# Kernel optimization log

Measured on AMD Instinct MI355X. Metric: run time of the kernel, lower is better.

## Reference

```python
import jax, jax.numpy as jnp
import numpy as np

CLASSES = (32, 32)
SUPERCLASSES = 8
OVERALL = CLASSES[0] * CLASSES[1]
CLASS_FACTOR = OVERALL // SUPERCLASSES


def lrelu(x):
    return jax.nn.leaky_relu(x, 0.01)


def conv1x1(x, w, b):
    # x: [B,C,H,W], w: [O,C], b: [O]
    return jnp.einsum('oc,bchw->bohw', w, x) + b[None, :, None, None]


def cond_mul(x, inds, W, b):
    # x: [N,I], inds: [N] int, W: [K,I,O], b: [K,O]
    return jnp.einsum('ni,nio->no', x, W[inds]) + b[inds]


def setup_inputs() -> dict:
    key = jax.random.key(0)
    ks = jax.random.split(key, 24)
    s = 0.05
    d = {}
    d['x_in'] = jax.random.normal(ks[0], (1, 128, 192, 256), dtype=jnp.float32)
    # mask branch
    d['Wm1'] = jax.random.normal(ks[1], (32, 128)) * s
    d['bm1'] = jnp.zeros((32,), jnp.float32)
    d['Wm2'] = jax.random.normal(ks[2], (16, 32)) * s
    d['bm2'] = jnp.zeros((16,), jnp.float32)
    d['Wm3'] = jax.random.normal(ks[3], (1, 16)) * s
    d['bm3'] = jnp.zeros((1,), jnp.float32)
    # classification branch
    d['Wcl1'] = jax.random.normal(ks[4], (128, 128)) * s
    d['bcl1'] = jnp.zeros((128,), jnp.float32)
    d['Wcl21'] = jax.random.normal(ks[5], (128, 128)) * s
    d['bcl21'] = jnp.zeros((128,), jnp.float32)
    d['Wcl31'] = jax.random.normal(ks[6], (32, 128)) * s
    d['bcl31'] = jnp.zeros((32,), jnp.float32)
    d['Wcl22'] = jax.random.normal(ks[7], (CLASSES[0], 128, 32)) * s  # CondMul
    d['bcl22'] = jnp.zeros((CLASSES[0], 32), jnp.float32)
    d['Wcl32'] = jax.random.normal(ks[8], (CLASSES[0], 32, CLASSES[1])) * s
    d['bcl32'] = jnp.zeros((CLASSES[0], CLASSES[1]), jnp.float32)
    d['Wr1'] = jax.random.normal(ks[9], (128, 128)) * s
    d['br1'] = jnp.zeros((128,), jnp.float32)
    d['Wr2'] = jax.random.normal(ks[10], (SUPERCLASSES, 128, 32)) * s
    d['br2'] = jnp.zeros((SUPERCLASSES, 32), jnp.float32)
    d['Wr3'] = jax.random.normal(ks[11], (OVERALL, 32, 1)) * s
    d['br3'] = jnp.zeros((OVERALL, 1), jnp.float32)
    return d


def reference(x_in, Wm1, bm1, Wm2, bm2, Wm3, bm3,
              Wcl1, bcl1, Wcl21, bcl21, Wcl31, bcl31,
              Wcl22, bcl22, Wcl32, bcl32,
              Wr1, br1, Wr2, br2, Wr3, br3):
    B = x_in.shape[0]
    # mask branch
    m = lrelu(conv1x1(x_in, Wm1, bm1))
    m = lrelu(conv1x1(m, Wm2, bm2))
    mask = lrelu(conv1x1(m, Wm3, bm3))
    # classification branch
    x = lrelu(conv1x1(x_in, Wcl1, bcl1))          # [B,128,H,W]
    # torch: transpose(1,3) -> [B,W,H,C], flatten
    x_l = jnp.transpose(x, (0, 3, 2, 1)).reshape(-1, x.shape[1])
    x2 = lrelu(conv1x1(x, Wcl21, bcl21))
    cl1 = conv1x1(x2, Wcl31, bcl31)               # [B,classes0,H,W]
    inds1 = jnp.argmax(cl1, axis=1).reshape(-1).astype(jnp.int32)  # [N] (B,H,W order)
    h = lrelu(cond_mul(x_l, inds1, Wcl22, bcl22))  # [N,32]
    h = cond_mul(h, inds1, Wcl32, bcl32)           # [N,classes1]
    inds2 = jnp.argmax(h, axis=1).astype(jnp.int32)
    inds = inds1 * CLASSES[1] + inds2
    inds_r = jnp.clip(inds, 0, OVERALL - 1).astype(jnp.int32)
    inds_super = jnp.clip(inds_r // CLASS_FACTOR, 0, SUPERCLASSES - 1)
    r = lrelu(conv1x1(x_in, Wr1, br1))
    r_l = jnp.transpose(r, (0, 3, 2, 1)).reshape(-1, r.shape[1])
    r2 = lrelu(cond_mul(r_l, inds_super, Wr2, br2))  # [N,32]
    regression = cond_mul(r2, inds_r, Wr3, br3)      # [N,1]
    regression = regression.reshape(B, 1, 1, -1)
    inds = inds.reshape(regression.shape)
    x_real = (inds.astype(jnp.float32) + regression) * (1.0 / float(OVERALL))
    return (x_real, mask)
```

## Files before the change

### kernel.cpp

```cpp
#include <hip/hip_runtime.h>

#define HH 192
#define WW 256
#define NPIX (HH*WW)
#define NSEG (NPIX/64)

__device__ __forceinline__ float lrelu(float v) { return v > 0.0f ? v : 0.01f * v; }

__global__ __launch_bounds__(256, 3) void k_fused1(
    const float* __restrict__ X,
    const float* __restrict__ Wcl1, const float* __restrict__ bcl1,
    const float* __restrict__ Wr1,  const float* __restrict__ br1,
    const float* __restrict__ Wm1,  const float* __restrict__ bm1,
    const float* __restrict__ Wm2,  const float* __restrict__ bm2,
    const float* __restrict__ Wm3,  const float* __restrict__ bm3,
    float* __restrict__ x_t, float* __restrict__ r_t,
    float* __restrict__ out)
{
    __shared__ float As[16][132];
    __shared__ float Ws[16][132];
    __shared__ float m1buf[128][33];
    const int tid = threadIdx.x;
    const int q0  = blockIdx.x * 128;

    if (blockIdx.y == 2) {
        const int tc = tid & 31;
        const int tr = tid >> 5;
        float acc[4][4];
        #pragma unroll
        for (int i = 0; i < 4; ++i)
            #pragma unroll
            for (int j = 0; j < 4; ++j)
                acc[i][j] = bm1[tr * 4 + j];

        for (int k0 = 0; k0 < 128; k0 += 16) {
            #pragma unroll
            for (int p = 0; p < 2; ++p) {
                int lin = p * 1024 + tid * 4;
                int kk = lin >> 7, px = lin & 127;
                float4 v = *(const float4*)(X + (k0 + kk) * NPIX + q0 + px);
                *(float4*)(&As[kk][px]) = v;
            }
            if (tid < 128) {
                int row = tid >> 2, kc = (tid & 3) * 4;
                float4 v = *(const float4*)(Wm1 + row * 128 + k0 + kc);
                Ws[kc + 0][row] = v.x; Ws[kc + 1][row] = v.y;
                Ws[kc + 2][row] = v.z; Ws[kc + 3][row] = v.w;
            }
            __syncthreads();
            #pragma unroll
            for (int kk = 0; kk < 16; ++kk) {
                float4 a = *(const float4*)(&As[kk][tc * 4]);
                float4 w = *(const float4*)(&Ws[kk][tr * 4]);
                float av[4] = {a.x,a.y,a.z,a.w};
                float wv[4] = {w.x,w.y,w.z,w.w};
                #pragma unroll
                for (int i = 0; i < 4; ++i)
                    #pragma unroll
                    for (int j = 0; j < 4; ++j)
                        acc[i][j] = fmaf(av[i], wv[j], acc[i][j]);
            }
            __syncthreads();
        }
        #pragma unroll
        for (int i = 0; i < 4; ++i)
            #pragma unroll
            for (int j = 0; j < 4; ++j)
                m1buf[tc * 4 + i][tr * 4 + j] = lrelu(acc[i][j]);
        __syncthreads();
        if (tid < 128) {
            float m3 = bm3[0];
            #pragma unroll 2
            for (int j = 0; j < 16; ++j) {
                float s = bm2[j];
                #pragma unroll
                for (int k = 0; k < 32; ++k)
                    s = fmaf(Wm2[j * 32 + k], m1buf[tid][k], s);
                m3 = fmaf(Wm3[j], lrelu(s), m3);
            }
            out[NPIX + q0 + tid] = lrelu(m3);
        }
        return;
    }

    const float* __restrict__ W    = (blockIdx.y == 0) ? Wcl1 : Wr1;
    const float* __restrict__ bias = (blockIdx.y == 0) ? bcl1 : br1;
    float* __restrict__ outp       = (blockIdx.y == 0) ? x_t : r_t;

    const int tc = tid & 15;
    const int tr = tid >> 4;

    float acc[8][8];
    #pragma unroll
    for (int i = 0; i < 8; ++i)
        #pragma unroll
        for (int j = 0; j < 8; ++j)
            acc[i][j] = bias[(j >> 2) * 64 + tr * 4 + (j & 3)];

    for (int k0 = 0; k0 < 128; k0 += 16) {
        #pragma unroll
        for (int p = 0; p < 2; ++p) {
            int lin = p * 1024 + tid * 4;
            int kk = lin >> 7, px = lin & 127;
            float4 v = *(const float4*)(X + (k0 + kk) * NPIX + q0 + px);
            *(float4*)(&As[kk][px]) = v;
        }
        #pragma unroll
        for (int p = 0; p < 2; ++p) {
            int lin = p * 1024 + tid * 4;
            int row = lin >> 4, kc = lin & 15;
            float4 v = *(const float4*)(W + row * 128 + k0 + kc);
            Ws[kc + 0][row] = v.x; Ws[kc + 1][row] = v.y;
            Ws[kc + 2][row] = v.z; Ws[kc + 3][row] = v.w;
        }
        __syncthreads();
        #pragma unroll
        for (int kk = 0; kk < 16; ++kk) {
            float4 a0 = *(const float4*)(&As[kk][tc * 4]);
            float4 a1 = *(const float4*)(&As[kk][64 + tc * 4]);
            float4 w0 = *(const float4*)(&Ws[kk][tr * 4]);
            float4 w1 = *(const float4*)(&Ws[kk][64 + tr * 4]);
            float av[8] = {a0.x,a0.y,a0.z,a0.w,a1.x,a1.y,a1.z,a1.w};
            float wv[8] = {w0.x,w0.y,w0.z,w0.w,w1.x,w1.y,w1.z,w1.w};
            #pragma unroll
            for (int i = 0; i < 8; ++i)
                #pragma unroll
                for (int j = 0; j < 8; ++j)
                    acc[i][j] = fmaf(av[i], wv[j], acc[i][j]);
        }
        __syncthreads();
    }

    #pragma unroll
    for (int i = 0; i < 8; ++i) {
        int px = (i >> 2) * 64 + tc * 4 + (i & 3);
        int q  = q0 + px;
        int np = (q & 255) * 192 + (q >> 8);
        float* op = outp + (size_t)np * 128;
        #pragma unroll
        for (int jg = 0; jg < 2; ++jg) {
            float4 o;
            o.x = lrelu(acc[i][jg*4+0]); o.y = lrelu(acc[i][jg*4+1]);
            o.z = lrelu(acc[i][jg*4+2]); o.w = lrelu(acc[i][jg*4+3]);
            *(float4*)(op + jg * 64 + tr * 4) = o;
        }
    }
}

__global__ __launch_bounds__(256, 2) void k1b(
    const float* __restrict__ x_t,
    const float* __restrict__ Wcl21, const float* __restrict__ bcl21,
    const float* __restrict__ Wcl31, const float* __restrict__ bcl31,
    int* __restrict__ inds1_q)
{
    __shared__ float smem[12672];
    float (*As)[132]     = (float(*)[132])smem;
    float (*Ws)[132]     = (float(*)[132])(smem + 2112);
    float (*W31)[132]    = (float(*)[132])smem;
    float (*x2t)[132]    = (float(*)[132])(smem + 4224);
    float (*cl1buf)[33]  = (float(*)[33]) (smem + 4224);

    const int tid = threadIdx.x;
    const int n0  = blockIdx.x * 128;
    const int tcA = tid & 15, trA = tid >> 4;
    const int tcB = tid & 31, trB = tid >> 5;

    float accB[4][4];
    #pragma unroll
    for (int i = 0; i < 4; ++i)
        #pragma unroll
        for (int j = 0; j < 4; ++j)
            accB[i][j] = bcl31[trB * 4 + j];

    for (int h = 0; h < 2; ++h) {
        float acc2[2][4][4];
        #pragma unroll
        for (int gi = 0; gi < 2; ++gi)
            #pragma unroll
            for (int i = 0; i < 4; ++i)
                #pragma unroll
                for (int j = 0; j < 4; ++j)
                    acc2[gi][i][j] = bcl21[h * 64 + trA * 4 + j];

        for (int k0 = 0; k0 < 128; k0 += 16) {
            #pragma unroll
            for (int p = 0; p < 2; ++p) {
                int lin = p * 1024 + tid * 4;
                int px = lin >> 4, kc = lin & 15;
                float4 v = *(const float4*)(x_t + (size_t)(n0 + px) * 128 + k0 + kc);
                As[kc + 0][px] = v.x; As[kc + 1][px] = v.y;
                As[kc + 2][px] = v.z; As[kc + 3][px] = v.w;
            }
            {
                int r = tid >> 2, kc = (tid & 3) * 4;
                float4 v = *(const float4*)(Wcl21 + (h * 64 + r) * 128 + k0 + kc);
                Ws[kc + 0][r] = v.x; Ws[kc + 1][r] = v.y;
                Ws[kc + 2][r] = v.z; Ws[kc + 3][r] = v.w;
            }
            __syncthreads();
            #pragma unroll
            for (int kk = 0; kk < 16; ++kk) {
                float4 a0 = *(const float4*)(&As[kk][tcA * 4]);
                float4 a1 = *(const float4*)(&As[kk][64 + tcA * 4]);
                float4 w  = *(const float4*)(&Ws[kk][trA * 4]);
                float av0[4] = {a0.x,a0.y,a0.z,a0.w};
                float av1[4] = {a1.x,a1.y,a1.z,a1.w};
                float wv[4]  = {w.x,w.y,w.z,w.w};
                #pragma unroll
                for (int i = 0; i < 4; ++i)
                    #pragma unroll
                    for (int j = 0; j < 4; ++j) {
                        acc2[0][i][j] = fmaf(av0[i], wv[j], acc2[0][i][j]);
                        acc2[1][i][j] = fmaf(av1[i], wv[j], acc2[1][i][j]);
                    }
            }
            __syncthreads();
        }
        #pragma unroll
        for (int j = 0; j < 4; ++j) {
            int row = trA * 4 + j;
            #pragma unroll
            for (int gi = 0; gi < 2; ++gi) {
                float4 o;
                o.x = lrelu(acc2[gi][0][j]); o.y = lrelu(acc2[gi][1][j]);
                o.z = lrelu(acc2[gi][2][j]); o.w = lrelu(acc2[gi][3][j]);
                *(float4*)(&x2t[row][gi * 64 + tcA * 4]) = o;
            }
        }
        __syncthreads();
        #pragma unroll
        for (int p = 0; p < 4; ++p) {
            int lin = p * 1024 + tid * 4;
            int row = lin >> 7, kc = lin & 127;
            *(float4*)(&W31[row][kc]) = *(const float4*)(Wcl31 + row * 128 + kc);
        }
        __syncthreads();
        for (int k = 0; k < 64; ++k) {
            float4 a = *(const float4*)(&x2t[k][tcB * 4]);
            float av[4] = {a.x,a.y,a.z,a.w};
            float wv[4];
            #pragma unroll
            for (int j = 0; j < 4; ++j) wv[j] = W31[trB * 4 + j][h * 64 + k];
            #pragma unroll
            for (int i = 0; i < 4; ++i)
                #pragma unroll
                for (int j = 0; j < 4; ++j)
                    accB[i][j] = fmaf(av[i], wv[j], accB[i][j]);
        }
        __syncthreads();
    }

    #pragma unroll
    for (int i = 0; i < 4; ++i)
        #pragma unroll
        for (int j = 0; j < 4; ++j)
            cl1buf[tcB * 4 + i][trB * 4 + j] = accB[i][j];
    __syncthreads();
    if (tid < 128) {
        float bv = cl1buf[tid][0]; int bi = 0;
        #pragma unroll
        for (int c = 1; c < 32; ++c) {
            float v = cl1buf[tid][c];
            if (v > bv) { bv = v; bi = c; }
        }
        int n = n0 + tid;
        int w = n / 192, hh = n - w * 192;
        inds1_q[hh * 256 + w] = bi;
    }
}

__global__ void k_hist(const int* __restrict__ inds1_q, int* __restrict__ bh) {
    int tid = threadIdx.x;
    int n = blockIdx.x * 256 + tid;
    int key = inds1_q[n];
    int lane = tid & 63;
    int cnt = 0;
    for (int k = 0; k < 32; ++k) {
        unsigned long long m = __ballot(key == k);
        if (lane == k) cnt = __popcll(m);
    }
    if (lane < 32) bh[(n >> 6) * 32 + lane] = cnt;
}

__global__ void k_scanA(const int* __restrict__ bh, int* __restrict__ ebb,
                        int* __restrict__ total) {
    __shared__ int s[256];
    const int k = blockIdx.x, t = threadIdx.x;
    int v0 = bh[(t * 3 + 0) * 32 + k];
    int v1 = bh[(t * 3 + 1) * 32 + k];
    int v2 = bh[(t * 3 + 2) * 32 + k];
    int sum = v0 + v1 + v2;
    s[t] = sum; __syncthreads();
    for (int d = 1; d < 256; d <<= 1) {
        int x = (t >= d) ? s[t - d] : 0;
        __syncthreads();
        s[t] += x;
        __syncthreads();
    }
    int ex = s[t] - sum;
    ebb[(t * 3 + 0) * 32 + k] = ex;
    ebb[(t * 3 + 1) * 32 + k] = ex + v0;
    ebb[(t * 3 + 2) * 32 + k] = ex + v0 + v1;
    if (t == 255) total[k] = s[255];
}

__global__ void k_scatter2(const int* __restrict__ inds1_q,
                           const int* __restrict__ ebb,
                           const int* __restrict__ total,
                           int* __restrict__ order)
{
    __shared__ int ttot[32];
    const int tid = threadIdx.x;
    if (tid < 32) ttot[tid] = total[tid];
    __syncthreads();
    int n = blockIdx.x * 256 + tid;
    int key = inds1_q[n];
    int lane = tid & 63;
    unsigned long long peers = 0;
    for (int k = 0; k < 32; ++k) {
        unsigned long long m = __ballot(key == k);
        if (key == k) peers = m;
    }
    int rank = __popcll(peers & ((1ull << lane) - 1ull));
    int cbase = 0;
    #pragma unroll
    for (int k = 0; k < 32; ++k) cbase += (k < key) ? ttot[k] : 0;
    order[cbase + ebb[(n >> 6) * 32 + key] + rank] = n;
}

__global__ __launch_bounds__(256, 4) void k2h(
    const float* __restrict__ x_t,
    const float* __restrict__ Wcl22, const float* __restrict__ bcl22,
    const float* __restrict__ Wcl32, const float* __restrict__ bcl32,
    const int* __restrict__ total, const int* __restrict__ order,
    int* __restrict__ ind_ord)
{
    __shared__ float Was[4096];
    __shared__ float Wbs[1024];
    __shared__ int cpre[33];
    __shared__ int cbase[33];
    __shared__ int ttot[32];

    const int tid = threadIdx.x;
    if (tid < 32) ttot[tid] = total[tid];
    __syncthreads();
    if (tid == 0) {
        int s = 0, cb = 0;
        for (int k = 0; k < 32; ++k) {
            cpre[k] = s; cbase[k] = cb;
            int c = ttot[k];
            s += (c + 255) >> 8;
            cb += c;
        }
        cpre[32] = s; cbase[32] = cb;
    }
    __syncthreads();
    const int ci = blockIdx.x;
    if (ci >= cpre[32]) return;
    int cls = 0;
    while (cpre[cls + 1] <= ci) ++cls;
    const int st   = (ci - cpre[cls]) * 256;
    const int npx  = min(256, ttot[cls] - st);
    const int base = cbase[cls] + st;

    {
        const float4* ws = (const float4*)(Wcl22 + cls * 4096);
        #pragma unroll
        for (int j = 0; j < 4; ++j) ((float4*)Was)[j * 256 + tid] = ws[j * 256 + tid];
        ((float4*)Wbs)[tid] = ((const float4*)(Wcl32 + cls * 1024))[tid];
    }
    __syncthreads();

    const int m = order[base + min(tid, npx - 1)];
    const float4* xp = (const float4*)(x_t + (size_t)m * 128);

    float h[32];
    #pragma unroll
    for (int j = 0; j < 32; ++j) h[j] = bcl22[cls * 32 + j];
    #pragma unroll 2
    for (int c4 = 0; c4 < 32; ++c4) {
        float4 xv = xp[c4];
        float xa[4] = {xv.x, xv.y, xv.z, xv.w};
        #pragma unroll
        for (int cc = 0; cc < 4; ++cc) {
            const float* wr = &Was[(c4 * 4 + cc) * 32];
            #pragma unroll
            for (int j = 0; j < 32; ++j) h[j] = fmaf(xa[cc], wr[j], h[j]);
        }
    }
    #pragma unroll
    for (int j = 0; j < 32; ++j) h[j] = lrelu(h[j]);

    float g[32];
    #pragma unroll
    for (int j = 0; j < 32; ++j) g[j] = bcl32[cls * 32 + j];
    #pragma unroll 2
    for (int c = 0; c < 32; ++c) {
        float hv = h[c];
        const float* wr = &Wbs[c * 32];
        #pragma unroll
        for (int j = 0; j < 32; ++j) g[j] = fmaf(hv, wr[j], g[j]);
    }
    float bv = g[0]; int bi = 0;
    #pragma unroll
    for (int j = 1; j < 32; ++j)
        if (g[j] > bv) { bv = g[j]; bi = j; }
    if (tid < npx) ind_ord[base + tid] = cls * 32 + bi;
}

__global__ __launch_bounds__(256, 4) void k2r(
    const float* __restrict__ r_t,
    const float* __restrict__ Wr2,  const float* __restrict__ br2,
    const float* __restrict__ Wr3,  const float* __restrict__ br3,
    const int* __restrict__ total, const int* __restrict__ order,
    const int* __restrict__ ind_ord,
    float* __restrict__ out)
{
    __shared__ float Wcs[4096];
    __shared__ int cpre[33];
    __shared__ int cbase[33];
    __shared__ int ttot[32];

    const int tid = threadIdx.x;
    if (tid < 32) ttot[tid] = total[tid];
    __syncthreads();
    if (tid == 0) {
        int s = 0, cb = 0;
        for (int k = 0; k < 32; ++k) {
            cpre[k] = s; cbase[k] = cb;
            int c = ttot[k];
            s += (c + 255) >> 8;
            cb += c;
        }
        cpre[32] = s; cbase[32] = cb;
    }
    __syncthreads();
    const int ci = blockIdx.x;
    if (ci >= cpre[32]) return;
    int cls = 0;
    while (cpre[cls + 1] <= ci) ++cls;
    const int st   = (ci - cpre[cls]) * 256;
    const int npx  = min(256, ttot[cls] - st);
    const int base = cbase[cls] + st;
    const int sup  = cls >> 2;

    {
        const float4* ws = (const float4*)(Wr2 + sup * 4096);
        #pragma unroll
        for (int j = 0; j < 4; ++j) ((float4*)Wcs)[j * 256 + tid] = ws[j * 256 + tid];
    }
    __syncthreads();

    const int li  = min(tid, npx - 1);
    const int m   = order[base + li];
    const int ind = ind_ord[base + li];
    const float4* rp = (const float4*)(r_t + (size_t)m * 128);

    float r2[32];
    #pragma unroll
    for (int j = 0; j < 32; ++j) r2[j] = br2[sup * 32 + j];
    #pragma unroll 2
    for (int c4 = 0; c4 < 32; ++c4) {
        float4 rv = rp[c4];
        float ra[4] = {rv.x, rv.y, rv.z, rv.w};
        #pragma unroll
        for (int cc = 0; cc < 4; ++cc) {
            const float* wr = &Wcs[(c4 * 4 + cc) * 32];
            #pragma unroll
            for (int j = 0; j < 32; ++j) r2[j] = fmaf(ra[cc], wr[j], r2[j]);
        }
    }

    float reg = br3[ind];
    const float* __restrict__ w3 = Wr3 + ind * 32;
    #pragma unroll
    for (int j = 0; j < 32; ++j) reg = fmaf(lrelu(r2[j]), w3[j], reg);

    if (tid < npx) out[m] = ((float)ind + reg) * (1.0f / 1024.0f);
}

extern "C" void kernel_launch(void* const* d_in, const int* in_sizes, int n_in,
                              void* d_out, int out_size, void* d_ws, size_t ws_size,
                              hipStream_t stream)
{
    const float* X     = (const float*)d_in[0];
    const float* Wm1   = (const float*)d_in[1];
    const float* bm1   = (const float*)d_in[2];
    const float* Wm2   = (const float*)d_in[3];
    const float* bm2   = (const float*)d_in[4];
    const float* Wm3   = (const float*)d_in[5];
    const float* bm3   = (const float*)d_in[6];
    const float* Wcl1  = (const float*)d_in[7];
    const float* bcl1  = (const float*)d_in[8];
    const float* Wcl21 = (const float*)d_in[9];
    const float* bcl21 = (const float*)d_in[10];
    const float* Wcl31 = (const float*)d_in[11];
    const float* bcl31 = (const float*)d_in[12];
    const float* Wcl22 = (const float*)d_in[13];
    const float* bcl22 = (const float*)d_in[14];
    const float* Wcl32 = (const float*)d_in[15];
    const float* bcl32 = (const float*)d_in[16];
    const float* Wr1   = (const float*)d_in[17];
    const float* br1   = (const float*)d_in[18];
    const float* Wr2   = (const float*)d_in[19];
    const float* br2   = (const float*)d_in[20];
    const float* Wr3   = (const float*)d_in[21];
    const float* br3   = (const float*)d_in[22];
    float* out = (float*)d_out;

    float* x_t   = (float*)d_ws;
    float* r_t   = x_t + (size_t)NPIX * 128;
    int* inds1_q = (int*)(r_t + (size_t)NPIX * 128);
    int* order   = inds1_q + NPIX;
    int* ind_ord = order + NPIX;
    int* bh      = ind_ord + NPIX;
    int* ebb     = bh + NSEG * 32;
    int* total   = ebb + NSEG * 32;

    k_fused1<<<dim3(NPIX / 128, 3), 256, 0, stream>>>(X, Wcl1, bcl1, Wr1, br1,
                                                      Wm1, bm1, Wm2, bm2, Wm3, bm3,
                                                      x_t, r_t, out);
    k1b<<<NPIX / 128, 256, 0, stream>>>(x_t, Wcl21, bcl21, Wcl31, bcl31, inds1_q);
    k_hist<<<NPIX / 256, 256, 0, stream>>>(inds1_q, bh);
    k_scanA<<<32, 256, 0, stream>>>(bh, ebb, total);
    k_scatter2<<<NPIX / 256, 256, 0, stream>>>(inds1_q, ebb, total, order);
    k2h<<<224, 256, 0, stream>>>(x_t, Wcl22, bcl22, Wcl32, bcl32, total, order, ind_ord);
    k2r<<<224, 256, 0, stream>>>(r_t, Wr2, br2, Wr3, br3, total, order, ind_ord, out);
}
```

Baseline: 246.3 us.

## Double-buffer fused conv GEMM tiles and merge classification/regression tail kernels

Measured after the change: 860.2 us. +249.2%, slower.

```diff
diff --git a/kernel.cpp b/kernel.cpp
--- a/kernel.cpp
+++ b/kernel.cpp
@@ -17,9 +17,13 @@
     float* __restrict__ x_t, float* __restrict__ r_t,
     float* __restrict__ out)
 {
-    __shared__ float As[16][132];
-    __shared__ float Ws[16][132];
-    __shared__ float m1buf[128][33];
+    __shared__ float smem[8448];
+    float (*A0)[132]  = (float(*)[132])(smem);
+    float (*A1)[132]  = (float(*)[132])(smem + 2112);
+    float (*W0)[132]  = (float(*)[132])(smem + 4224);
+    float (*W1)[132]  = (float(*)[132])(smem + 6336);
+    float (*m1buf)[33] = (float(*)[33])(smem + 2112);
+
     const int tid = threadIdx.x;
     const int q0  = blockIdx.x * 128;
 
@@ -38,20 +42,20 @@
             for (int p = 0; p < 2; ++p) {
                 int lin = p * 1024 + tid * 4;
                 int kk = lin >> 7, px = lin & 127;
-                float4 v = *(const float4*)(X + (k0 + kk) * NPIX + q0 + px);
-                *(float4*)(&As[kk][px]) = v;
+                float4 v = *(const float4*)(X + (size_t)(k0 + kk) * NPIX + q0 + px);
+                *(float4*)(&A0[kk][px]) = v;
             }
             if (tid < 128) {
                 int row = tid >> 2, kc = (tid & 3) * 4;
                 float4 v = *(const float4*)(Wm1 + row * 128 + k0 + kc);
-                Ws[kc + 0][row] = v.x; Ws[kc + 1][row] = v.y;
-                Ws[kc + 2][row] = v.z; Ws[kc + 3][row] = v.w;
+                W0[kc + 0][row] = v.x; W0[kc + 1][row] = v.y;
+                W0[kc + 2][row] = v.z; W0[kc + 3][row] = v.w;
             }
             __syncthreads();
             #pragma unroll
             for (int kk = 0; kk < 16; ++kk) {
-                float4 a = *(const float4*)(&As[kk][tc * 4]);
-                float4 w = *(const float4*)(&Ws[kk][tr * 4]);
+                float4 a = *(const float4*)(&A0[kk][tc * 4]);
+                float4 w = *(const float4*)(&W0[kk][tr * 4]);
                 float av[4] = {a.x,a.y,a.z,a.w};
                 float wv[4] = {w.x,w.y,w.z,w.w};
                 #pragma unroll
@@ -90,6 +94,17 @@
     const int tc = tid & 15;
     const int tr = tid >> 4;
 
+    const int lin0 = tid * 4,        lin1 = 1024 + tid * 4;
+    const int akk0 = lin0 >> 7, apx0 = lin0 & 127;
+    const int akk1 = lin1 >> 7, apx1 = lin1 & 127;
+    const int wr0  = lin0 >> 4, wkc0 = lin0 & 15;
+    const int wr1_ = lin1 >> 4, wkc1 = lin1 & 15;
+
+    const float* Xp0 = X + (size_t)akk0 * NPIX + q0 + apx0;
+    const float* Xp1 = X + (size_t)akk1 * NPIX + q0 + apx1;
+    const float* Wp0 = W + wr0  * 128 + wkc0;
+    const float* Wp1 = W + wr1_ * 128 + wkc1;
+
     float acc[8][8];
     #pragma unroll
     for (int i = 0; i < 8; ++i)
@@ -97,29 +112,35 @@
         for (int j = 0; j < 8; ++j)
             acc[i][j] = bias[(j >> 2) * 64 + tr * 4 + (j & 3)];
 
+    float (*Ac)[132] = A0; float (*An)[132] = A1;
+    float (*Wc)[132] = W0; float (*Wn)[132] = W1;
+
+    float4 ra0 = *(const float4*)(Xp0);
+    float4 ra1 = *(const float4*)(Xp1);
+    float4 rw0 = *(const float4*)(Wp0);
+    float4 rw1 = *(const float4*)(Wp1);
+    *(float4*)(&Ac[akk0][apx0]) = ra0;
+    *(float4*)(&Ac[akk1][apx1]) = ra1;
+    Wc[wkc0 + 0][wr0 ] = rw0.x; Wc[wkc0 + 1][wr0 ] = rw0.y;
+    Wc[wkc0 + 2][wr0 ] = rw0.z; Wc[wkc0 + 3][wr0 ] = rw0.w;
+    Wc[wkc1 + 0][wr1_] = rw1.x; Wc[wkc1 + 1][wr1_] = rw1.y;
+    Wc[wkc1 + 2][wr1_] = rw1.z; Wc[wkc1 + 3][wr1_] = rw1.w;
+    __syncthreads();
+
+    #pragma unroll 2
     for (int k0 = 0; k0 < 128; k0 += 16) {
-        #pragma unroll
-        for (int p = 0; p < 2; ++p) {
-            int lin = p * 1024 + tid * 4;
-            int kk = lin >> 7, px = lin & 127;
-            float4 v = *(const float4*)(X + (k0 + kk) * NPIX + q0 + px);
-            *(float4*)(&As[kk][px]) = v;
-        }
-        #pragma unroll
-        for (int p = 0; p < 2; ++p) {
-            int lin = p * 1024 + tid * 4;
-            int row = lin >> 4, kc = lin & 15;
-            float4 v = *(const float4*)(W + row * 128 + k0 + kc);
-            Ws[kc + 0][row] = v.x; Ws[kc + 1][row] = v.y;
-            Ws[kc + 2][row] = v.z; Ws[kc + 3][row] = v.w;
-        }
-        __syncthreads();
+        if (k0 < 112) {
+            ra0 = *(const float4*)(Xp0 + (size_t)(k0 + 16) * NPIX);
+            ra1 = *(const float4*)(Xp1 + (size_t)(k0 + 16) * NPIX);
+            rw0 = *(const float4*)(Wp0 + (k0 + 16));
+            rw1 = *(const float4*)(Wp1 + (k0 + 16));
+        }
         #pragma unroll
         for (int kk = 0; kk < 16; ++kk) {
-            float4 a0 = *(const float4*)(&As[kk][tc * 4]);
-            float4 a1 = *(const float4*)(&As[kk][64 + tc * 4]);
-            float4 w0 = *(const float4*)(&Ws[kk][tr * 4]);
-            float4 w1 = *(const float4*)(&Ws[kk][64 + tr * 4]);
+            float4 a0 = *(const float4*)(&Ac[kk][tc * 4]);
+            float4 a1 = *(const float4*)(&Ac[kk][64 + tc * 4]);
+            float4 w0 = *(const float4*)(&Wc[kk][tr * 4]);
+            float4 w1 = *(const float4*)(&Wc[kk][64 + tr * 4]);
             float av[8] = {a0.x,a0.y,a0.z,a0.w,a1.x,a1.y,a1.z,a1.w};
             float wv[8] = {w0.x,w0.y,w0.z,w0.w,w1.x,w1.y,w1.z,w1.w};
             #pragma unroll
@@ -128,7 +149,18 @@
                 for (int j = 0; j < 8; ++j)
                     acc[i][j] = fmaf(av[i], wv[j], acc[i][j]);
         }
-        __syncthreads();
+        if (k0 < 112) {
+            *(float4*)(&An[akk0][apx0]) = ra0;
+            *(float4*)(&An[akk1][apx1]) = ra1;
+            Wn[wkc0 + 0][wr0 ] = rw0.x; Wn[wkc0 + 1][wr0 ] = rw0.y;
+            Wn[wkc0 + 2][wr0 ] = rw0.z; Wn[wkc0 + 3][wr0 ] = rw0.w;
+            Wn[wkc1 + 0][wr1_] = rw1.x; Wn[wkc1 + 1][wr1_] = rw1.y;
+            Wn[wkc1 + 2][wr1_] = rw1.z; Wn[wkc1 + 3][wr1_] = rw1.w;
+        }
+        __syncthreads();
+        float (*t)[132];
+        t = Ac; Ac = An; An = t;
+        t = Wc; Wc = Wn; Wn = t;
     }
 
     #pragma unroll
@@ -328,15 +360,18 @@
     order[cbase + ebb[(n >> 6) * 32 + key] + rank] = n;
 }
 
-__global__ __launch_bounds__(256, 4) void k2h(
-    const float* __restrict__ x_t,
+__global__ __launch_bounds__(256, 4) void k2hr(
+    const float* __restrict__ x_t, const float* __restrict__ r_t,
     const float* __restrict__ Wcl22, const float* __restrict__ bcl22,
     const float* __restrict__ Wcl32, const float* __restrict__ bcl32,
+    const float* __restrict__ Wr2,  const float* __restrict__ br2,
+    const float* __restrict__ Wr3,  const float* __restrict__ br3,
     const int* __restrict__ total, const int* __restrict__ order,
-    int* __restrict__ ind_ord)
+    float* __restrict__ out)
 {
     __shared__ float Was[4096];
     __shared__ float Wbs[1024];
+    __shared__ float Wcs[4096];
     __shared__ int cpre[33];
     __shared__ int cbase[33];
     __shared__ int ttot[32];
@@ -362,16 +397,22 @@
     const int st   = (ci - cpre[cls]) * 256;
     const int npx  = min(256, ttot[cls] - st);
     const int base = cbase[cls] + st;
+    const int sup  = cls >> 2;
 
     {
-        const float4* ws = (const float4*)(Wcl22 + cls * 4096);
-        #pragma unroll
-        for (int j = 0; j < 4; ++j) ((float4*)Was)[j * 256 + tid] = ws[j * 256 + tid];
+        const float4* wa = (const float4*)(Wcl22 + cls * 4096);
+        const float4* wc = (const float4*)(Wr2 + sup * 4096);
+        #pragma unroll
+        for (int j = 0; j < 4; ++j) {
+            ((float4*)Was)[j * 256 + tid] = wa[j * 256 + tid];
+            ((float4*)Wcs)[j * 256 + tid] = wc[j * 256 + tid];
+        }
         ((float4*)Wbs)[tid] = ((const float4*)(Wcl32 + cls * 1024))[tid];
     }
     __syncthreads();
 
-    const int m = order[base + min(tid, npx - 1)];
+    const int li = min(tid, npx - 1);
+    const int m  = order[base + li];
     const float4* xp = (const float4*)(x_t + (size_t)m * 128);
 
     float h[32];
@@ -405,57 +446,9 @@
     #pragma unroll
     for (int j = 1; j < 32; ++j)
         if (g[j] > bv) { bv = g[j]; bi = j; }
-    if (tid < npx) ind_ord[base + tid] = cls * 32 + bi;
-}
-
-__global__ __launch_bounds__(256, 4) void k2r(
-    const float* __restrict__ r_t,
-    const float* __restrict__ Wr2,  const float* __restrict__ br2,
-    const float* __restrict__ Wr3,  const float* __restrict__ br3,
-    const int* __restrict__ total, const int* __restrict__ order,
-    const int* __restrict__ ind_ord,
-    float* __restrict__ out)
-{
-    __shared__ float Wcs[4096];
-    __shared__ int cpre[33];
-    __shared__ int cbase[33];
-    __shared__ int ttot[32];
-
-    const int tid = threadIdx.x;
-    if (tid < 32) ttot[tid] = total[tid];
-    __syncthreads();
-    if (tid == 0) {
-        int s = 0, cb = 0;
-        for (int k = 0; k < 32; ++k) {
-            cpre[k] = s; cbase[k] = cb;
-            int c = ttot[k];
-            s += (c + 255) >> 8;
-            cb += c;
-        }
-        cpre[32] = s; cbase[32] = cb;
-    }
-    __syncthreads();
-    const int ci = blockIdx.x;
-    if (ci >= cpre[32]) return;
-    int cls = 0;
-    while (cpre[cls + 1] <= ci) ++cls;
-    const int st   = (ci - cpre[cls]) * 256;
-    const int npx  = min(256, ttot[cls] - st);
-    const int base = cbase[cls] + st;
-    const int sup  = cls >> 2;
-
-    {
-        const float4* ws = (const float4*)(Wr2 + sup * 4096);
-        #pragma unroll
-        for (int j = 0; j < 4; ++j) ((float4*)Wcs)[j * 256 + tid] = ws[j * 256 + tid];
-    }
-    __syncthreads();
-
-    const int li  = min(tid, npx - 1);
-    const int m   = order[base + li];
-    const int ind = ind_ord[base + li];
+    const int ind = cls * 32 + bi;
+
     const float4* rp = (const float4*)(r_t + (size_t)m * 128);
-
     float r2[32];
     #pragma unroll
     for (int j = 0; j < 32; ++j) r2[j] = br2[sup * 32 + j];
@@ -524,6 +517,6 @@
     k_hist<<<NPIX / 256, 256, 0, stream>>>(inds1_q, bh);
     k_scanA<<<32, 256, 0, stream>>>(bh, ebb, total);
     k_scatter2<<<NPIX / 256, 256, 0, stream>>>(inds1_q, ebb, total, order);
-    k2h<<<224, 256, 0, stream>>>(x_t, Wcl22, bcl22, Wcl32, bcl32, total, order, ind_ord);
-    k2r<<<224, 256, 0, stream>>>(r_t, Wr2, br2, Wr3, br3, total, order, ind_ord, out);
-}
+    k2hr<<<224, 256, 0, stream>>>(x_t, r_t, Wcl22, bcl22, Wcl32, bcl32,
+                                  Wr2, br2, Wr3, br3, total, order, out);
+}
```

## Double-buffer k_fused1 tiles with direct global-to-LDS async loads

Applied to the files above, without the earlier changes.

Result: slower. 513.7 us (+108.6%).

```diff
diff --git a/kernel.cpp b/kernel.cpp
--- a/kernel.cpp
+++ b/kernel.cpp
@@ -7,66 +7,145 @@
 
 __device__ __forceinline__ float lrelu(float v) { return v > 0.0f ? v : 0.01f * v; }
 
+#define GAS1(p) (const __attribute__((address_space(1))) void*)(p)
+#define LAS3(p) (__attribute__((address_space(3))) void*)(p)
+
+__global__ void k_tw(const float* __restrict__ Wc, const float* __restrict__ Wr,
+                     const float* __restrict__ Wm,
+                     float* __restrict__ Wct, float* __restrict__ Wrt,
+                     float* __restrict__ Wmt)
+{
+    const int b = blockIdx.x, tid = threadIdx.x;
+    const float* __restrict__ src = (b == 0) ? Wc : (b == 1) ? Wr : Wm;
+    float* __restrict__ dst       = (b == 0) ? Wct : (b == 1) ? Wrt : Wmt;
+    const int olog = (b == 2) ? 5 : 7;
+    const int n    = 128 << olog;
+    for (int idx = tid; idx < n; idx += 256) {
+        int k = idx >> olog, o = idx & ((1 << olog) - 1);
+        dst[idx] = src[o * 128 + k];
+    }
+}
+
 __global__ __launch_bounds__(256, 3) void k_fused1(
     const float* __restrict__ X,
-    const float* __restrict__ Wcl1, const float* __restrict__ bcl1,
-    const float* __restrict__ Wr1,  const float* __restrict__ br1,
-    const float* __restrict__ Wm1,  const float* __restrict__ bm1,
+    const float* __restrict__ Wct,  const float* __restrict__ bcl1,
+    const float* __restrict__ Wrt,  const float* __restrict__ br1,
+    const float* __restrict__ Wmt,  const float* __restrict__ bm1,
     const float* __restrict__ Wm2,  const float* __restrict__ bm2,
     const float* __restrict__ Wm3,  const float* __restrict__ bm3,
     float* __restrict__ x_t, float* __restrict__ r_t,
     float* __restrict__ out)
 {
-    __shared__ float As[16][132];
-    __shared__ float Ws[16][132];
-    __shared__ float m1buf[128][33];
+    __shared__ float smem[8192];
+    float (*As0)[128] = (float(*)[128])(smem);
+    float (*Ws0)[128] = (float(*)[128])(smem + 2048);
+    float (*As1)[128] = (float(*)[128])(smem + 4096);
+    float (*Ws1)[128] = (float(*)[128])(smem + 6144);
+    float (*m1buf)[33] = (float(*)[33])smem;
+
     const int tid = threadIdx.x;
+    const int l   = tid & 63;
+    const int wv  = tid >> 6;
     const int q0  = blockIdx.x * 128;
 
+#define STAGE_MAIN(Ab, Wb, Wsrc, kb) do {                                     \
+    int c_ = 2 * wv;                                                          \
+    int row0_ = 2 * c_ + (l >> 5);                                            \
+    int col_  = (l & 31) * 4;                                                 \
+    __builtin_amdgcn_global_load_lds(                                         \
+        GAS1(X + (size_t)((kb) + row0_) * NPIX + q0 + col_),                  \
+        LAS3(&Ab[0][0] + c_ * 256), 16, 0, 0);                                \
+    __builtin_amdgcn_global_load_lds(                                         \
+        GAS1(Wsrc + ((kb) + row0_) * 128 + col_),                             \
+        LAS3(&Wb[0][0] + c_ * 256), 16, 0, 0);                                \
+    int row1_ = row0_ + 2;                                                    \
+    __builtin_amdgcn_global_load_lds(                                         \
+        GAS1(X + (size_t)((kb) + row1_) * NPIX + q0 + col_),                  \
+        LAS3(&Ab[0][0] + c_ * 256 + 256), 16, 0, 0);                          \
+    __builtin_amdgcn_global_load_lds(                                         \
+        GAS1(Wsrc + ((kb) + row1_) * 128 + col_),                             \
+        LAS3(&Wb[0][0] + c_ * 256 + 256), 16, 0, 0);                          \
+} while (0)
+
+#define COMPUTE_MAIN(Ab, Wb) do {                                             \
+    _Pragma("unroll")                                                         \
+    for (int kk = 0; kk < 16; ++kk) {                                         \
+        float4 a0 = *(const float4*)(&Ab[kk][tc * 4]);                        \
+        float4 a1 = *(const float4*)(&Ab[kk][64 + tc * 4]);                   \
+        float4 w0 = *(const float4*)(&Wb[kk][tr * 4]);                        \
+        float4 w1 = *(const float4*)(&Wb[kk][64 + tr * 4]);                   \
+        float av[8] = {a0.x,a0.y,a0.z,a0.w,a1.x,a1.y,a1.z,a1.w};              \
+        float wvv[8] = {w0.x,w0.y,w0.z,w0.w,w1.x,w1.y,w1.z,w1.w};             \
+        _Pragma("unroll")                                                     \
+        for (int i = 0; i < 8; ++i)                                           \
+            _Pragma("unroll")                                                 \
+            for (int j = 0; j < 8; ++j)                                       \
+                acc[i][j] = fmaf(av[i], wvv[j], acc[i][j]);                   \
+    }                                                                         \
+} while (0)
+
     if (blockIdx.y == 2) {
-        const int tc = tid & 31;
-        const int tr = tid >> 5;
-        float acc[4][4];
+        float (*Wm0)[32] = (float(*)[32])(smem + 2048);
+        float (*Wm1b)[32] = (float(*)[32])(smem + 6144);
+        const int mc = tid & 31;
+        const int mr = tid >> 5;
+        float accM[4][4];
         #pragma unroll
         for (int i = 0; i < 4; ++i)
             #pragma unroll
             for (int j = 0; j < 4; ++j)
-                acc[i][j] = bm1[tr * 4 + j];
-
-        for (int k0 = 0; k0 < 128; k0 += 16) {
-            #pragma unroll
-            for (int p = 0; p < 2; ++p) {
-                int lin = p * 1024 + tid * 4;
-                int kk = lin >> 7, px = lin & 127;
-                float4 v = *(const float4*)(X + (k0 + kk) * NPIX + q0 + px);
-                *(float4*)(&As[kk][px]) = v;
-            }
-            if (tid < 128) {
-                int row = tid >> 2, kc = (tid & 3) * 4;
-                float4 v = *(const float4*)(Wm1 + row * 128 + k0 + kc);
-                Ws[kc + 0][row] = v.x; Ws[kc + 1][row] = v.y;
-                Ws[kc + 2][row] = v.z; Ws[kc + 3][row] = v.w;
-            }
+                accM[i][j] = bm1[mr * 4 + j];
+
+#define STAGE_MASK(Ab, Wmb, kb) do {                                          \
+    int c_ = 2 * wv;                                                          \
+    int row0_ = 2 * c_ + (l >> 5);                                            \
+    int col_  = (l & 31) * 4;                                                 \
+    __builtin_amdgcn_global_load_lds(                                         \
+        GAS1(X + (size_t)((kb) + row0_) * NPIX + q0 + col_),                  \
+        LAS3(&Ab[0][0] + c_ * 256), 16, 0, 0);                                \
+    int row1_ = row0_ + 2;                                                    \
+    __builtin_amdgcn_global_load_lds(                                         \
+        GAS1(X + (size_t)((kb) + row1_) * NPIX + q0 + col_),                  \
+        LAS3(&Ab[0][0] + c_ * 256 + 256), 16, 0, 0);                          \
+    if (wv < 2) {                                                             \
+        int mrow_ = wv * 8 + (l >> 3);                                        \
+        int mcol_ = (l & 7) * 4;                                              \
+        __builtin_amdgcn_global_load_lds(                                     \
+            GAS1(Wmt + ((kb) + mrow_) * 32 + mcol_),                          \
+            LAS3(&Wmb[0][0] + wv * 256), 16, 0, 0);                           \
+    }                                                                         \
+} while (0)
+
+#define COMPUTE_MASK(Ab, Wmb) do {                                            \
+    _Pragma("unroll")                                                         \
+    for (int kk = 0; kk < 16; ++kk) {                                         \
+        float4 a = *(const float4*)(&Ab[kk][mc * 4]);                         \
+        float4 w = *(const float4*)(&Wmb[kk][mr * 4]);                        \
+        float av[4] = {a.x,a.y,a.z,a.w};                                      \
+        float wvv[4] = {w.x,w.y,w.z,w.w};                                     \
+        _Pragma("unroll")                                                     \
+        for (int i = 0; i < 4; ++i)                                           \
+            _Pragma("unroll")                                                 \
+            for (int j = 0; j < 4; ++j)                                       \
+                accM[i][j] = fmaf(av[i], wvv[j], accM[i][j]);                 \
+    }                                                                         \
+} while (0)
+
+        STAGE_MASK(As0, Wm0, 0);
+        __syncthreads();
+        for (int k0 = 0; k0 < 128; k0 += 32) {
+            if (k0 + 16 < 128) STAGE_MASK(As1, Wm1b, k0 + 16);
+            COMPUTE_MASK(As0, Wm0);
             __syncthreads();
-            #pragma unroll
-            for (int kk = 0; kk < 16; ++kk) {
-                float4 a = *(const float4*)(&As[kk][tc * 4]);
-                float4 w = *(const float4*)(&Ws[kk][tr * 4]);
-                float av[4] = {a.x,a.y,a.z,a.w};
-                float wv[4] = {w.x,w.y,w.z,w.w};
-                #pragma unroll
-                for (int i = 0; i < 4; ++i)
-                    #pragma unroll
-                    for (int j = 0; j < 4; ++j)
-                        acc[i][j] = fmaf(av[i], wv[j], acc[i][j]);
-            }
+            if (k0 + 32 < 128) STAGE_MASK(As0, Wm0, k0 + 32);
+            COMPUTE_MASK(As1, Wm1b);
             __syncthreads();
         }
         #pragma unroll
         for (int i = 0; i < 4; ++i)
             #pragma unroll
             for (int j = 0; j < 4; ++j)
-                m1buf[tc * 4 + i][tr * 4 + j] = lrelu(acc[i][j]);
+                m1buf[mc * 4 + i][mr * 4 + j] = lrelu(accM[i][j]);
         __syncthreads();
         if (tid < 128) {
             float m3 = bm3[0];
@@ -83,7 +162,7 @@
         return;
     }
 
-    const float* __restrict__ W    = (blockIdx.y == 0) ? Wcl1 : Wr1;
+    const float* __restrict__ Wt   = (blockIdx.y == 0) ? Wct : Wrt;
     const float* __restrict__ bias = (blockIdx.y == 0) ? bcl1 : br1;
     float* __restrict__ outp       = (blockIdx.y == 0) ? x_t : r_t;
 
@@ -97,37 +176,14 @@
         for (int j = 0; j < 8; ++j)
             acc[i][j] = bias[(j >> 2) * 64 + tr * 4 + (j & 3)];
 
-    for (int k0 = 0; k0 < 128; k0 += 16) {
-        #pragma unroll
-        for (int p = 0; p < 2; ++p) {
-            int lin = p * 1024 + tid * 4;
-            int kk = lin >> 7, px = lin & 127;
-            float4 v = *(const float4*)(X + (k0 + kk) * NPIX + q0 + px);
-            *(float4*)(&As[kk][px]) = v;
-        }
-        #pragma unroll
-        for (int p = 0; p < 2; ++p) {
-            int lin = p * 1024 + tid * 4;
-            int row = lin >> 4, kc = lin & 15;
-            float4 v = *(const float4*)(W + row * 128 + k0 + kc);
-            Ws[kc + 0][row] = v.x; Ws[kc + 1][row] = v.y;
-            Ws[kc + 2][row] = v.z; Ws[kc + 3][row] = v.w;
-        }
-        __syncthreads();
-        #pragma unroll
-        for (int kk = 0; kk < 16; ++kk) {
-            float4 a0 = *(const float4*)(&As[kk][tc * 4]);
-            float4 a1 = *(const float4*)(&As[kk][64 + tc * 4]);
-            float4 w0 = *(const float4*)(&Ws[kk][tr * 4]);
-            float4 w1 = *(const float4*)(&Ws[kk][64 + tr * 4]);
-            float av[8] = {a0.x,a0.y,a0.z,a0.w,a1.x,a1.y,a1.z,a1.w};
-            float wv[8] = {w0.x,w0.y,w0.z,w0.w,w1.x,w1.y,w1.z,w1.w};
-            #pragma unroll
-            for (int i = 0; i < 8; ++i)
-                #pragma unroll
-                for (int j = 0; j < 8; ++j)
-                    acc[i][j] = fmaf(av[i], wv[j], acc[i][j]);
-        }
+    STAGE_MAIN(As0, Ws0, Wt, 0);
+    __syncthreads();
+    for (int k0 = 0; k0 < 128; k0 += 32) {
+        if (k0 + 16 < 128) STAGE_MAIN(As1, Ws1, Wt, k0 + 16);
+        COMPUTE_MAIN(As0, Ws0);
+        __syncthreads();
+        if (k0 + 32 < 128) STAGE_MAIN(As0, Ws0, Wt, k0 + 32);
+        COMPUTE_MAIN(As1, Ws1);
         __syncthreads();
     }
 
@@ -516,9 +572,13 @@
     int* bh      = ind_ord + NPIX;
     int* ebb     = bh + NSEG * 32;
     int* total   = ebb + NSEG * 32;
-
-    k_fused1<<<dim3(NPIX / 128, 3), 256, 0, stream>>>(X, Wcl1, bcl1, Wr1, br1,
-                                                      Wm1, bm1, Wm2, bm2, Wm3, bm3,
+    float* Wct   = (float*)bh;
+    float* Wrt   = Wct + 16384;
+    float* Wmt   = Wrt + 16384;
+
+    k_tw<<<3, 256, 0, stream>>>(Wcl1, Wr1, Wm1, Wct, Wrt, Wmt);
+    k_fused1<<<dim3(NPIX / 128, 3), 256, 0, stream>>>(X, Wct, bcl1, Wrt, br1,
+                                                      Wmt, bm1, Wm2, bm2, Wm3, bm3,
                                                       x_t, r_t, out);
     k1b<<<NPIX / 128, 256, 0, stream>>>(x_t, Wcl21, bcl21, Wcl31, bcl31, inds1_q);
     k_hist<<<NPIX / 256, 256, 0, stream>>>(inds1_q, bh);
```

## Compute all 128 cl21 outputs in one K pass with 8x8 register tiles

Applied to the files above, without the earlier changes.

Result: no change. 241.9 us (-1.8%).

```diff
diff --git a/kernel.cpp b/kernel.cpp
--- a/kernel.cpp
+++ b/kernel.cpp
@@ -165,6 +165,48 @@
     const int tcA = tid & 15, trA = tid >> 4;
     const int tcB = tid & 31, trB = tid >> 5;
 
+    float acc[8][8];
+    #pragma unroll
+    for (int i = 0; i < 8; ++i)
+        #pragma unroll
+        for (int j = 0; j < 8; ++j)
+            acc[i][j] = bcl21[(j >> 2) * 64 + trA * 4 + (j & 3)];
+
+    for (int k0 = 0; k0 < 128; k0 += 16) {
+        #pragma unroll
+        for (int p = 0; p < 2; ++p) {
+            int lin = p * 1024 + tid * 4;
+            int px = lin >> 4, kc = lin & 15;
+            float4 v = *(const float4*)(x_t + (size_t)(n0 + px) * 128 + k0 + kc);
+            As[kc + 0][px] = v.x; As[kc + 1][px] = v.y;
+            As[kc + 2][px] = v.z; As[kc + 3][px] = v.w;
+        }
+        #pragma unroll
+        for (int p = 0; p < 2; ++p) {
+            int lin = p * 256 + tid;
+            int r = lin >> 2, kc = (lin & 3) * 4;
+            float4 v = *(const float4*)(Wcl21 + r * 128 + k0 + kc);
+            Ws[kc + 0][r] = v.x; Ws[kc + 1][r] = v.y;
+            Ws[kc + 2][r] = v.z; Ws[kc + 3][r] = v.w;
+        }
+        __syncthreads();
+        #pragma unroll
+        for (int kk = 0; kk < 16; ++kk) {
+            float4 a0 = *(const float4*)(&As[kk][tcA * 4]);
+            float4 a1 = *(const float4*)(&As[kk][64 + tcA * 4]);
+            float4 w0 = *(const float4*)(&Ws[kk][trA * 4]);
+            float4 w1 = *(const float4*)(&Ws[kk][64 + trA * 4]);
+            float av[8] = {a0.x,a0.y,a0.z,a0.w,a1.x,a1.y,a1.z,a1.w};
+            float wv[8] = {w0.x,w0.y,w0.z,w0.w,w1.x,w1.y,w1.z,w1.w};
+            #pragma unroll
+            for (int i = 0; i < 8; ++i)
+                #pragma unroll
+                for (int j = 0; j < 8; ++j)
+                    acc[i][j] = fmaf(av[i], wv[j], acc[i][j]);
+        }
+        __syncthreads();
+    }
+
     float accB[4][4];
     #pragma unroll
     for (int i = 0; i < 4; ++i)
@@ -172,83 +214,62 @@
         for (int j = 0; j < 4; ++j)
             accB[i][j] = bcl31[trB * 4 + j];
 
-    for (int h = 0; h < 2; ++h) {
-        float acc2[2][4][4];
-        #pragma unroll
-        for (int gi = 0; gi < 2; ++gi)
-            #pragma unroll
-            for (int i = 0; i < 4; ++i)
-                #pragma unroll
-                for (int j = 0; j < 4; ++j)
-                    acc2[gi][i][j] = bcl21[h * 64 + trA * 4 + j];
-
-        for (int k0 = 0; k0 < 128; k0 += 16) {
-            #pragma unroll
-            for (int p = 0; p < 2; ++p) {
-                int lin = p * 1024 + tid * 4;
-                int px = lin >> 4, kc = lin & 15;
-                float4 v = *(const float4*)(x_t + (size_t)(n0 + px) * 128 + k0 + kc);
-                As[kc + 0][px] = v.x; As[kc + 1][px] = v.y;
-                As[kc + 2][px] = v.z; As[kc + 3][px] = v.w;
-            }
-            {
-                int r = tid >> 2, kc = (tid & 3) * 4;
-                float4 v = *(const float4*)(Wcl21 + (h * 64 + r) * 128 + k0 + kc);
-                Ws[kc + 0][r] = v.x; Ws[kc + 1][r] = v.y;
-                Ws[kc + 2][r] = v.z; Ws[kc + 3][r] = v.w;
-            }
-            __syncthreads();
-            #pragma unroll
-            for (int kk = 0; kk < 16; ++kk) {
-                float4 a0 = *(const float4*)(&As[kk][tcA * 4]);
-                float4 a1 = *(const float4*)(&As[kk][64 + tcA * 4]);
-                float4 w  = *(const float4*)(&Ws[kk][trA * 4]);
-                float av0[4] = {a0.x,a0.y,a0.z,a0.w};
-                float av1[4] = {a1.x,a1.y,a1.z,a1.w};
-                float wv[4]  = {w.x,w.y,w.z,w.w};
-                #pragma unroll
-                for (int i = 0; i < 4; ++i)
-                    #pragma unroll
-                    for (int j = 0; j < 4; ++j) {
-                        acc2[0][i][j] = fmaf(av0[i], wv[j], acc2[0][i][j]);
-                        acc2[1][i][j] = fmaf(av1[i], wv[j], acc2[1][i][j]);
-                    }
-            }
-            __syncthreads();
-        }
-        #pragma unroll
-        for (int j = 0; j < 4; ++j) {
-            int row = trA * 4 + j;
-            #pragma unroll
-            for (int gi = 0; gi < 2; ++gi) {
-                float4 o;
-                o.x = lrelu(acc2[gi][0][j]); o.y = lrelu(acc2[gi][1][j]);
-                o.z = lrelu(acc2[gi][2][j]); o.w = lrelu(acc2[gi][3][j]);
-                *(float4*)(&x2t[row][gi * 64 + tcA * 4]) = o;
-            }
-        }
-        __syncthreads();
-        #pragma unroll
-        for (int p = 0; p < 4; ++p) {
-            int lin = p * 1024 + tid * 4;
-            int row = lin >> 7, kc = lin & 127;
-            *(float4*)(&W31[row][kc]) = *(const float4*)(Wcl31 + row * 128 + kc);
-        }
-        __syncthreads();
-        for (int k = 0; k < 64; ++k) {
-            float4 a = *(const float4*)(&x2t[k][tcB * 4]);
-            float av[4] = {a.x,a.y,a.z,a.w};
-            float wv[4];
-            #pragma unroll
-            for (int j = 0; j < 4; ++j) wv[j] = W31[trB * 4 + j][h * 64 + k];
-            #pragma unroll
-            for (int i = 0; i < 4; ++i)
-                #pragma unroll
-                for (int j = 0; j < 4; ++j)
-                    accB[i][j] = fmaf(av[i], wv[j], accB[i][j]);
-        }
-        __syncthreads();
-    }
+    #pragma unroll
+    for (int p = 0; p < 4; ++p) {
+        int lin = p * 1024 + tid * 4;
+        int row = lin >> 7, kc = lin & 127;
+        *(float4*)(&W31[row][kc]) = *(const float4*)(Wcl31 + row * 128 + kc);
+    }
+    #pragma unroll
+    for (int j = 0; j < 4; ++j) {
+        int row = trA * 4 + j;
+        #pragma unroll
+        for (int gi = 0; gi < 2; ++gi) {
+            float4 o;
+            o.x = lrelu(acc[gi*4+0][j]); o.y = lrelu(acc[gi*4+1][j]);
+            o.z = lrelu(acc[gi*4+2][j]); o.w = lrelu(acc[gi*4+3][j]);
+            *(float4*)(&x2t[row][gi * 64 + tcA * 4]) = o;
+        }
+    }
+    __syncthreads();
+    for (int k = 0; k < 64; ++k) {
+        float4 a = *(const float4*)(&x2t[k][tcB * 4]);
+        float av[4] = {a.x,a.y,a.z,a.w};
+        float wv[4];
+        #pragma unroll
+        for (int j = 0; j < 4; ++j) wv[j] = W31[trB * 4 + j][k];
+        #pragma unroll
+        for (int i = 0; i < 4; ++i)
+            #pragma unroll
+            for (int j = 0; j < 4; ++j)
+                accB[i][j] = fmaf(av[i], wv[j], accB[i][j]);
+    }
+    __syncthreads();
+    #pragma unroll
+    for (int j = 0; j < 4; ++j) {
+        int row = trA * 4 + j;
+        #pragma unroll
+        for (int gi = 0; gi < 2; ++gi) {
+            float4 o;
+            o.x = lrelu(acc[gi*4+0][4+j]); o.y = lrelu(acc[gi*4+1][4+j]);
+            o.z = lrelu(acc[gi*4+2][4+j]); o.w = lrelu(acc[gi*4+3][4+j]);
+            *(float4*)(&x2t[row][gi * 64 + tcA * 4]) = o;
+        }
+    }
+    __syncthreads();
+    for (int k = 0; k < 64; ++k) {
+        float4 a = *(const float4*)(&x2t[k][tcB * 4]);
+        float av[4] = {a.x,a.y,a.z,a.w};
+        float wv[4];
+        #pragma unroll
+        for (int j = 0; j < 4; ++j) wv[j] = W31[trB * 4 + j][64 + k];
+        #pragma unroll
+        for (int i = 0; i < 4; ++i)
+            #pragma unroll
+            for (int j = 0; j < 4; ++j)
+                accB[i][j] = fmaf(av[i], wv[j], accB[i][j]);
+    }
+    __syncthreads();
 
     #pragma unroll
     for (int i = 0; i < 4; ++i)
```
